# Kernel tuning notes

Hardware: AMD Instinct MI355X
Metric: run time of the kernel (lower is better)

## Reference

```python
import jax, jax.numpy as jnp
import numpy as np

H = 128
NH = 8
HD = H // NH  # 16
TANH_ALPHA = 10.0
LN_EPS = 1e-5


def _layer_norm(x, g, b):
    mu = jnp.mean(x, axis=-1, keepdims=True)
    var = jnp.mean((x - mu) ** 2, axis=-1, keepdims=True)
    return (x - mu) / jnp.sqrt(var + LN_EPS) * g + b


def setup_inputs() -> dict:
    key = jax.random.key(0)
    ks = jax.random.split(key, 24)
    B, N = 1024, 500

    def p(k, shape):
        return jax.random.normal(k, shape, dtype=jnp.float32) * 0.05

    inp = {
        "node_embeddings": jax.random.normal(ks[0], (B, N, H), jnp.float32),
        "graph_embeddings": jax.random.normal(ks[1], (B, H), jnp.float32),
        "first_node": jax.random.randint(ks[2], (B,), 0, N, jnp.int32),
        "current_node": jax.random.randint(ks[3], (B,), 0, N, jnp.int32),
        "mask": jax.random.randint(ks[4], (B, N), 0, 2, jnp.int32),
        # linear_first: Linear(384, 128)
        "W_first": p(ks[5], (H, 3 * H)),
        "b_first": p(ks[6], (H,)),
        # ln1 / ln2
        "g1": jnp.ones((H,), jnp.float32),
        "beta1": jnp.zeros((H,), jnp.float32),
        "g2": jnp.ones((H,), jnp.float32),
        "beta2": jnp.zeros((H,), jnp.float32),
        # LSTM(128,128) single layer, gate order i,f,g,o
        "W_ih": p(ks[7], (4 * H, H)),
        "W_hh": p(ks[8], (4 * H, H)),
        "b_ih": p(ks[9], (4 * H,)),
        "b_hh": p(ks[10], (4 * H,)),
        # attention / output projections (no bias)
        "Wq": p(ks[11], (H, H)),
        "Wk": p(ks[12], (H, H)),
        "Wv": p(ks[13], (H, H)),
        "Wproj": p(ks[14], (H, H)),
        # logitk: Linear(128,128) with bias
        "Wlk": p(ks[15], (H, H)),
        "blk": p(ks[16], (H,)),
    }
    return inp


def reference(node_embeddings, graph_embeddings, W_first, b_first, g1, beta1,
              W_ih, W_hh, b_ih, b_hh, g2, beta2, Wq, Wk, Wv, Wproj, Wlk, blk,
              first_node, current_node, mask):
    B, N, _ = node_embeddings.shape
    dt = node_embeddings.dtype

    # build_cache: K/V/logitK projections of all node embeddings
    ck = node_embeddings @ Wk.T                # [B,N,128]
    cv = node_embeddings @ Wv.T                # [B,N,128]
    lk = node_embeddings @ Wlk.T + blk         # [B,N,128]

    # context construction
    bidx = jnp.arange(B)
    first_emb = node_embeddings[bidx, first_node]    # [B,128]
    cur_emb = node_embeddings[bidx, current_node]    # [B,128]
    context = jnp.concatenate([graph_embeddings, first_emb, cur_emb], axis=1)
    context = _layer_norm(context @ W_first.T + b_first, g1, beta1)

    # single LSTM step from zero state (build_cache resets h,c to 0)
    gates = context @ W_ih.T + b_ih + b_hh           # h_prev = 0 -> no W_hh term
    i, f, g, o = jnp.split(gates, 4, axis=-1)
    c = jax.nn.sigmoid(i) * jnp.tanh(g)              # c_prev = 0
    h = jax.nn.sigmoid(o) * jnp.tanh(c)
    ctx = _layer_norm(h, g2, beta2)

    # multi-head single-query attention; note (e h) split: head is the FAST dim
    q = (ctx @ Wq.T).reshape(B, HD, NH).transpose(0, 2, 1)       # [B,h,e]
    k = ck.reshape(B, N, HD, NH).transpose(0, 3, 1, 2)           # [B,h,N,e]
    v = cv.reshape(B, N, HD, NH).transpose(0, 3, 1, 2)           # [B,h,N,e]
    maskf = mask.astype(dt)
    scores = jnp.einsum('bhe,bhne->bhn', q, k) / np.sqrt(HD) + maskf[:, None, :]
    att = jax.nn.softmax(scores, axis=-1)
    oh = jnp.einsum('bhn,bhne->bhe', att, v)                     # [B,h,e]
    att_out = oh.reshape(B, H)                                   # (h e): h slow, e fast

    context_emb = att_out @ Wproj.T                              # [B,128]
    comp = jnp.einsum('be,bne->bn', lk, context_emb[:, None, :].squeeze(1)[:, :][None].squeeze(0) if False else context_emb) if False else jnp.einsum('bne,be->bn', lk, context_emb)
    comp = comp / np.sqrt(H)
    comp = TANH_ALPHA * jnp.tanh(comp)
    out = jnp.where(mask == 1, -jnp.inf, comp)
    return out
```

## Files before the change

kernel.cpp:

```cpp
#include <hip/hip_runtime.h>
#include <math.h>

#define NBATCH 1024
#define NNODE  500
#define HDIM   128
#define NHEAD  8
#define G1K    2
#define SPLIT  2
#define CPB    4
#define CHUNK  64
#define PSTRIDE 1056
#define RSQRT_H 0.08838834764831845f
#define MASK_NEG (-1e30f)

__device__ __forceinline__ float wave_sum64(float v) {
    #pragma unroll
    for (int off = 32; off >= 1; off >>= 1) v += __shfl_xor(v, off, 64);
    return v;
}
__device__ __forceinline__ float wave_max64(float v) {
    #pragma unroll
    for (int off = 32; off >= 1; off >>= 1) v = fmaxf(v, __shfl_xor(v, off, 64));
    return v;
}

template<int G>
__device__ __forceinline__ void block_ln(float (&x)[G], const float* __restrict__ gw,
                                         const float* __restrict__ bw,
                                         int t, int lane, int wv, float (*wpart)[G])
{
    float s[G];
    #pragma unroll
    for (int g = 0; g < G; ++g) s[g] = x[g];
    #pragma unroll
    for (int off = 32; off >= 1; off >>= 1) {
        #pragma unroll
        for (int g = 0; g < G; ++g) s[g] += __shfl_xor(s[g], off, 64);
    }
    if (lane == 0) {
        #pragma unroll
        for (int g = 0; g < G; ++g) wpart[wv][g] = s[g];
    }
    __syncthreads();
    float mu[G];
    #pragma unroll
    for (int g = 0; g < G; ++g) mu[g] = (wpart[0][g] + wpart[1][g]) * (1.f/128.f);
    __syncthreads();
    #pragma unroll
    for (int g = 0; g < G; ++g) { float d = x[g] - mu[g]; s[g] = d * d; }
    #pragma unroll
    for (int off = 32; off >= 1; off >>= 1) {
        #pragma unroll
        for (int g = 0; g < G; ++g) s[g] += __shfl_xor(s[g], off, 64);
    }
    if (lane == 0) {
        #pragma unroll
        for (int g = 0; g < G; ++g) wpart[wv][g] = s[g];
    }
    __syncthreads();
    float gv = gw[t], bv = bw[t];
    #pragma unroll
    for (int g = 0; g < G; ++g) {
        float var = (wpart[0][g] + wpart[1][g]) * (1.f/128.f);
        x[g] = (x[g] - mu[g]) / sqrtf(var + 1e-5f) * gv + bv;
    }
    __syncthreads();
}

__global__ __launch_bounds__(128) void k1_context(
    const float* __restrict__ node, const float* __restrict__ graph,
    const int* __restrict__ firstn, const int* __restrict__ curn,
    const float* __restrict__ W_first, const float* __restrict__ b_first,
    const float* __restrict__ g1, const float* __restrict__ beta1,
    const float* __restrict__ W_ih, const float* __restrict__ b_ih,
    const float* __restrict__ b_hh, const float* __restrict__ g2,
    const float* __restrict__ beta2, const float* __restrict__ Wq,
    const float* __restrict__ Wk, float* __restrict__ qW_out)
{
    const int t = threadIdx.x;
    const int lane = t & 63, wv = t >> 6;
    const int b0 = blockIdx.x * G1K;
    __shared__ __align__(16) float ctx[G1K][384];
    __shared__ __align__(16) float bufB[G1K][128];
    __shared__ float wpart[2][G1K];

    #pragma unroll
    for (int g = 0; g < G1K; ++g) {
        int b = b0 + g;
        ctx[g][t]       = graph[b*HDIM + t];
        ctx[g][128 + t] = node[((size_t)b*NNODE + firstn[b])*HDIM + t];
        ctx[g][256 + t] = node[((size_t)b*NNODE + curn[b])*HDIM + t];
    }
    __syncthreads();

    float x[G1K];
    {
        const float4* Wf4 = (const float4*)W_first;
        float bf = b_first[t];
        #pragma unroll
        for (int g = 0; g < G1K; ++g) x[g] = bf;
        for (int j4 = 0; j4 < 96; ++j4) {
            float4 w = Wf4[t*96 + j4];
            #pragma unroll
            for (int g = 0; g < G1K; ++g) {
                float4 c = ((const float4*)ctx[g])[j4];
                x[g] += c.x*w.x + c.y*w.y + c.z*w.z + c.w*w.w;
            }
        }
    }
    block_ln<G1K>(x, g1, beta1, t, lane, wv, wpart);

    #pragma unroll
    for (int g = 0; g < G1K; ++g) bufB[g][t] = x[g];
    __syncthreads();

    float gi[G1K], gg[G1K], go[G1K];
    {
        const float4* Wih4 = (const float4*)W_ih;
        float bi = b_ih[t]       + b_hh[t];
        float bg = b_ih[256 + t] + b_hh[256 + t];
        float bo = b_ih[384 + t] + b_hh[384 + t];
        #pragma unroll
        for (int g = 0; g < G1K; ++g) { gi[g] = bi; gg[g] = bg; go[g] = bo; }
        for (int j4 = 0; j4 < 32; ++j4) {
            float4 wi = Wih4[(size_t)t*32 + j4];
            float4 wg = Wih4[(size_t)(256 + t)*32 + j4];
            float4 wo = Wih4[(size_t)(384 + t)*32 + j4];
            #pragma unroll
            for (int g = 0; g < G1K; ++g) {
                float4 v = ((const float4*)bufB[g])[j4];
                gi[g] += v.x*wi.x + v.y*wi.y + v.z*wi.z + v.w*wi.w;
                gg[g] += v.x*wg.x + v.y*wg.y + v.z*wg.z + v.w*wg.w;
                go[g] += v.x*wo.x + v.y*wo.y + v.z*wo.z + v.w*wo.w;
            }
        }
    }
    #pragma unroll
    for (int g = 0; g < G1K; ++g) {
        float ig = 1.f / (1.f + expf(-gi[g]));
        float cc = ig * tanhf(gg[g]);
        float og = 1.f / (1.f + expf(-go[g]));
        x[g] = og * tanhf(cc);
    }
    block_ln<G1K>(x, g2, beta2, t, lane, wv, wpart);

    #pragma unroll
    for (int g = 0; g < G1K; ++g) bufB[g][t] = x[g];
    __syncthreads();

    float q8[G1K];
    #pragma unroll
    for (int g = 0; g < G1K; ++g) q8[g] = 0.f;
    {
        const float4* Wq4 = (const float4*)Wq;
        for (int j4 = 0; j4 < 32; ++j4) {
            float4 w = Wq4[t*32 + j4];
            #pragma unroll
            for (int g = 0; g < G1K; ++g) {
                float4 v = ((const float4*)bufB[g])[j4];
                q8[g] += v.x*w.x + v.y*w.y + v.z*w.z + v.w*w.w;
            }
        }
    }
    __syncthreads();
    #pragma unroll
    for (int g = 0; g < G1K; ++g) bufB[g][t] = q8[g];
    __syncthreads();

    for (int h = 0; h < NHEAD; ++h) {
        float a[G1K];
        #pragma unroll
        for (int g = 0; g < G1K; ++g) a[g] = 0.f;
        for (int e = 0; e < 16; ++e) {
            float w = Wk[(e*8 + h)*HDIM + t];
            #pragma unroll
            for (int g = 0; g < G1K; ++g) a[g] += bufB[g][e*8 + h] * w;
        }
        #pragma unroll
        for (int g = 0; g < G1K; ++g)
            qW_out[((size_t)(b0 + g)*NHEAD + h)*HDIM + t] = 0.25f * a[g];
    }
}

__global__ __launch_bounds__(256) void k2a_reg(
    const float* __restrict__ node, const int* __restrict__ mask,
    const float* __restrict__ qW, float* __restrict__ part)
{
    const int b   = blockIdx.x >> 1;
    const int s   = blockIdx.x & (SPLIT - 1);
    const int tid = threadIdx.x;
    const int lane = tid & 63;
    const int wave = tid >> 6;
    const int nbase = s * (CPB * CHUNK);

    const int rn = tid >> 2;
    const int dq = tid & 3;
    const int sg = tid >> 5;
    const int aq = tid & 31;

    __shared__ __align__(16) float4 s_tile[CHUNK*32];
    __shared__ __align__(16) float  s_qw[NHEAD*HDIM];
    __shared__ float s_p[NHEAD*CHUNK];
    __shared__ float s_mask[CHUNK];
    __shared__ float s_m[NHEAD], s_l[NHEAD], s_c[NHEAD];

    const float* nodeb = node + (size_t)b*NNODE*HDIM;
    const int*   maskb = mask + (size_t)b*NNODE;

    float4 R[8];
    {
        int gn = nbase + rn;
        if (gn < NNODE) {
            const float4* src = (const float4*)(nodeb + (size_t)gn*HDIM) + dq*8;
            #pragma unroll
            for (int k = 0; k < 8; ++k) R[k] = src[k];
        } else {
            #pragma unroll
            for (int k = 0; k < 8; ++k) R[k] = make_float4(0.f,0.f,0.f,0.f);
        }
    }
    ((float4*)s_qw)[tid] = ((const float4*)(qW + (size_t)b*NHEAD*HDIM))[tid];
    if (tid < CHUNK) {
        int gn = nbase + tid;
        s_mask[tid] = (gn < NNODE) ? (float)maskb[gn] : 0.f;
    }
    if (tid < NHEAD) { s_m[tid] = -INFINITY; s_l[tid] = 0.f; }

    float4 acc[NHEAD];
    #pragma unroll
    for (int h = 0; h < NHEAD; ++h) acc[h] = make_float4(0.f,0.f,0.f,0.f);

    __syncthreads();

    for (int ck = 0; ck < CPB; ++ck) {
        const int base = nbase + ck*CHUNK;

        {
            float sc[NHEAD];
            #pragma unroll
            for (int h = 0; h < NHEAD; ++h) {
                const float4* qh = (const float4*)(s_qw + h*HDIM) + dq*8;
                float t0 = 0.f;
                #pragma unroll
                for (int k = 0; k < 8; ++k) {
                    float4 w = qh[k];
                    t0 += R[k].x*w.x + R[k].y*w.y + R[k].z*w.z + R[k].w*w.w;
                }
                sc[h] = t0;
            }
            #pragma unroll
            for (int h = 0; h < NHEAD; ++h) {
                sc[h] += __shfl_xor(sc[h], 1, 64);
                sc[h] += __shfl_xor(sc[h], 2, 64);
            }
            if (dq == 0) {
                int gn = base + rn;
                float mf = s_mask[rn];
                bool oob = (gn >= NNODE);
                #pragma unroll
                for (int h = 0; h < NHEAD; ++h)
                    s_p[h*64 + rn] = oob ? -INFINITY : sc[h] + mf;
            }
        }
        #pragma unroll
        for (int k = 0; k < 8; ++k) {
            int q = dq*8 + k;
            s_tile[rn*32 + (q ^ (rn & 31))] = R[k];
        }
        __syncthreads();

        for (int hh = wave; hh < NHEAD; hh += 4) {
            float sv = s_p[hh*64 + lane];
            float mx = wave_max64(sv);
            float mO = s_m[hh];
            float mN = fmaxf(mO, mx);
            float pv = __expf(sv - mN);
            s_p[hh*64 + lane] = pv;
            float sm = wave_sum64(pv);
            if (lane == 0) {
                float corr = __expf(mO - mN);
                s_c[hh] = corr;
                s_l[hh] = s_l[hh]*corr + sm;
                s_m[hh] = mN;
            }
        }
        __syncthreads();

        if (ck + 1 < CPB) {
            int gn = base + CHUNK + rn;
            if (gn < NNODE) {
                const float4* src = (const float4*)(nodeb + (size_t)gn*HDIM) + dq*8;
                #pragma unroll
                for (int k = 0; k < 8; ++k) R[k] = src[k];
            } else {
                #pragma unroll
                for (int k = 0; k < 8; ++k) R[k] = make_float4(0.f,0.f,0.f,0.f);
            }
            if (tid < CHUNK) {
                int gm = base + CHUNK + tid;
                s_mask[tid] = (gm < NNODE) ? (float)maskb[gm] : 0.f;
            }
        }

        {
            #pragma unroll
            for (int h = 0; h < NHEAD; ++h) {
                float c = s_c[h];
                acc[h].x *= c; acc[h].y *= c; acc[h].z *= c; acc[h].w *= c;
            }
            #pragma unroll
            for (int j = 0; j < 8; ++j) {
                int n = sg*8 + j;
                float4 nv = s_tile[n*32 + (aq ^ (n & 31))];
                #pragma unroll
                for (int h = 0; h < NHEAD; ++h) {
                    float p = s_p[h*64 + n];
                    acc[h].x += p*nv.x; acc[h].y += p*nv.y;
                    acc[h].z += p*nv.z; acc[h].w += p*nv.w;
                }
            }
        }
        __syncthreads();
    }

    float* pbase = part + (size_t)blockIdx.x * PSTRIDE;
    #pragma unroll
    for (int h = 0; h < NHEAD; ++h) s_tile[(sg*8 + h)*32 + aq] = acc[h];
    if (tid < NHEAD) { pbase[tid] = s_m[tid]; pbase[8 + tid] = s_l[tid]; }
    __syncthreads();
    {
        const int h2 = tid >> 5, q2 = tid & 31;
        float4 tot = make_float4(0.f,0.f,0.f,0.f);
        #pragma unroll
        for (int ss = 0; ss < 8; ++ss) {
            float4 v = s_tile[(ss*8 + h2)*32 + q2];
            tot.x += v.x; tot.y += v.y; tot.z += v.z; tot.w += v.w;
        }
        *(float4*)(pbase + 16 + h2*HDIM + q2*4) = tot;
    }
}

__global__ __launch_bounds__(256) void k2b_reduce(
    const float* __restrict__ part, const float* __restrict__ Wv,
    const float* __restrict__ Wproj, const float* __restrict__ Wlk,
    const float* __restrict__ blk, float* __restrict__ wce_out,
    float* __restrict__ bias_out)
{
    const int b = blockIdx.x;
    const int tid = threadIdx.x;
    __shared__ __align__(16) float s_an[NHEAD*HDIM];
    __shared__ float s_ao[HDIM], s_ce[HDIM];

    {
        const int h = tid >> 5, q = tid & 31;
        const float* pb = part + (size_t)b*SPLIT*PSTRIDE;
        float m[SPLIT], l[SPLIT];
        float gm = -INFINITY;
        #pragma unroll
        for (int s = 0; s < SPLIT; ++s) {
            m[s] = pb[s*PSTRIDE + h];
            l[s] = pb[s*PSTRIDE + 8 + h];
            gm = fmaxf(gm, m[s]);
        }
        float lsum = 0.f;
        float4 tot = make_float4(0.f,0.f,0.f,0.f);
        #pragma unroll
        for (int s = 0; s < SPLIT; ++s) {
            float f = __expf(m[s] - gm);
            lsum += l[s] * f;
            float4 v = *(const float4*)(pb + s*PSTRIDE + 16 + h*HDIM + q*4);
            tot.x += f*v.x; tot.y += f*v.y; tot.z += f*v.z; tot.w += f*v.w;
        }
        float inv = 1.f / lsum;
        tot.x *= inv; tot.y *= inv; tot.z *= inv; tot.w *= inv;
        *(float4*)(s_an + h*HDIM + q*4) = tot;
    }
    __syncthreads();

    if (tid < HDIM) {
        const int c = tid, h = c >> 4, e = c & 15;
        const int row = e*8 + h;
        float oh = 0.f;
        for (int d = 0; d < HDIM; ++d) oh += s_an[h*HDIM + d] * Wv[row*HDIM + d];
        s_ao[c] = oh;
    }
    __syncthreads();
    if (tid < HDIM) {
        const int c = tid;
        float ce = 0.f;
        for (int j = 0; j < HDIM; ++j) ce += s_ao[j] * Wproj[c*HDIM + j];
        s_ce[c] = ce;
    }
    __syncthreads();
    if (tid < HDIM) {
        const int d = tid;
        float w = 0.f;
        for (int c = 0; c < HDIM; ++c) w += s_ce[c] * Wlk[c*HDIM + d];
        wce_out[(size_t)b*HDIM + d] = w * RSQRT_H;
        if (d == 0) {
            float bb = 0.f;
            for (int c = 0; c < HDIM; ++c) bb += s_ce[c] * blk[c];
            bias_out[b] = bb * RSQRT_H;
        }
    }
}

__global__ __launch_bounds__(256) void k2_flash_mono(
    const float* __restrict__ node, const int* __restrict__ mask,
    const float* __restrict__ qW, const float* __restrict__ Wv,
    const float* __restrict__ Wproj, const float* __restrict__ Wlk,
    const float* __restrict__ blk, float* __restrict__ wce_out,
    float* __restrict__ bias_out)
{
    const int b = blockIdx.x;
    const int tid = threadIdx.x;
    const int lane = tid & 63;
    const int wave = tid >> 6;

    __shared__ float4 s_tile[64*32];
    __shared__ __align__(16) float s_qw[NHEAD*HDIM];
    __shared__ float  s_p[NHEAD*64];
    __shared__ float  s_m[NHEAD], s_l[NHEAD], s_c[NHEAD];
    __shared__ float  s_ao[HDIM], s_ce[HDIM];

    ((float4*)s_qw)[tid] = ((const float4*)(qW + (size_t)b*NHEAD*HDIM))[tid];
    if (tid < NHEAD) { s_m[tid] = -INFINITY; s_l[tid] = 0.f; }

    float4 acc[NHEAD];
    #pragma unroll
    for (int h = 0; h < NHEAD; ++h) acc[h] = make_float4(0.f,0.f,0.f,0.f);

    const int sn = tid & 63;
    const int hp = tid >> 6;
    const int sg = tid >> 5;
    const int aq = tid & 31;
    const float* nodeb = node + (size_t)b*NNODE*HDIM;

    for (int tile = 0; tile < 8; ++tile) {
        const int base = tile*64;
        #pragma unroll
        for (int i = 0; i < 8; ++i) {
            int idx = i*256 + tid;
            int r = idx >> 5, qq = idx & 31;
            int gn = base + r;
            float4 v = make_float4(0.f,0.f,0.f,0.f);
            if (gn < NNODE) v = *(const float4*)(nodeb + (size_t)gn*HDIM + qq*4);
            s_tile[r*32 + (qq ^ (r & 31))] = v;
        }
        __syncthreads();
        {
            float s0 = 0.f, s1 = 0.f;
            const int rb = sn*32, sw = sn & 31;
            const float4* qa = (const float4*)(s_qw + hp*HDIM);
            const float4* qb = (const float4*)(s_qw + (hp + 4)*HDIM);
            #pragma unroll 8
            for (int qq = 0; qq < 32; ++qq) {
                float4 nv = s_tile[rb + (qq ^ sw)];
                float4 av = qa[qq];
                float4 bv = qb[qq];
                s0 += nv.x*av.x + nv.y*av.y + nv.z*av.z + nv.w*av.w;
                s1 += nv.x*bv.x + nv.y*bv.y + nv.z*bv.z + nv.w*bv.w;
            }
            int gn = base + sn;
            if (gn < NNODE) {
                float mf = (float)mask[(size_t)b*NNODE + gn];
                s0 += mf; s1 += mf;
            } else { s0 = -INFINITY; s1 = -INFINITY; }
            s_p[hp*64 + sn] = s0;
            s_p[(hp + 4)*64 + sn] = s1;
        }
        __syncthreads();
        for (int hh = wave; hh < NHEAD; hh += 4) {
            float sv = s_p[hh*64 + lane];
            float mx = wave_max64(sv);
            float mO = s_m[hh];
            float mN = fmaxf(mO, mx);
            float pv = __expf(sv - mN);
            s_p[hh*64 + lane] = pv;
            float sm = wave_sum64(pv);
            if (lane == 0) {
                float corr = __expf(mO - mN);
                s_c[hh] = corr;
                s_l[hh] = s_l[hh]*corr + sm;
                s_m[hh] = mN;
            }
        }
        __syncthreads();
        {
            #pragma unroll
            for (int h = 0; h < NHEAD; ++h) {
                float c = s_c[h];
                acc[h].x *= c; acc[h].y *= c; acc[h].z *= c; acc[h].w *= c;
            }
            #pragma unroll
            for (int j = 0; j < 8; ++j) {
                int n = sg*8 + j;
                float4 nv = s_tile[n*32 + (aq ^ (n & 31))];
                #pragma unroll
                for (int h = 0; h < NHEAD; ++h) {
                    float p = s_p[h*64 + n];
                    acc[h].x += p*nv.x; acc[h].y += p*nv.y;
                    acc[h].z += p*nv.z; acc[h].w += p*nv.w;
                }
            }
        }
        __syncthreads();
    }
    #pragma unroll
    for (int h = 0; h < NHEAD; ++h) s_tile[(sg*8 + h)*32 + aq] = acc[h];
    __syncthreads();
    {
        const int h2 = tid >> 5, q2 = tid & 31;
        float4 tot = make_float4(0.f,0.f,0.f,0.f);
        #pragma unroll
        for (int s = 0; s < 8; ++s) {
            float4 v = s_tile[(s*8 + h2)*32 + q2];
            tot.x += v.x; tot.y += v.y; tot.z += v.z; tot.w += v.w;
        }
        float inv = 1.f / s_l[h2];
        tot.x *= inv; tot.y *= inv; tot.z *= inv; tot.w *= inv;
        ((float4*)s_qw)[h2*32 + q2] = tot;
    }
    __syncthreads();
    if (tid < HDIM) {
        const int c = tid, h = c >> 4, e = c & 15;
        const int row = e*8 + h;
        float oh = 0.f;
        for (int d = 0; d < HDIM; ++d) oh += s_qw[h*HDIM + d] * Wv[row*HDIM + d];
        s_ao[c] = oh;
    }
    __syncthreads();
    if (tid < HDIM) {
        const int c = tid;
        float ce = 0.f;
        for (int j = 0; j < HDIM; ++j) ce += s_ao[j] * Wproj[c*HDIM + j];
        s_ce[c] = ce;
    }
    __syncthreads();
    if (tid < HDIM) {
        const int d = tid;
        float w = 0.f;
        for (int c = 0; c < HDIM; ++c) w += s_ce[c] * Wlk[c*HDIM + d];
        wce_out[(size_t)b*HDIM + d] = w * RSQRT_H;
        if (d == 0) {
            float bb = 0.f;
            for (int c = 0; c < HDIM; ++c) bb += s_ce[c] * blk[c];
            bias_out[b] = bb * RSQRT_H;
        }
    }
}

__global__ __launch_bounds__(256) void k3_out(
    const float* __restrict__ node, const int* __restrict__ mask,
    const float* __restrict__ wce, const float* __restrict__ biasv,
    float* __restrict__ out)
{
    const int slot = (int)((blockIdx.x*256u + threadIdx.x) >> 5);
    const int q = threadIdx.x & 31;
    const int b = slot / NNODE;
    const float4 nv = *(const float4*)(node + (size_t)slot*HDIM + q*4);
    const float4 wv = *(const float4*)(wce + (size_t)b*HDIM + q*4);
    float p = nv.x*wv.x + nv.y*wv.y + nv.z*wv.z + nv.w*wv.w;
    #pragma unroll
    for (int off = 16; off >= 1; off >>= 1) p += __shfl_xor(p, off, 32);
    if (q == 0) {
        float v = 10.f * tanhf(p + biasv[b]);
        out[slot] = (mask[slot] == 1) ? MASK_NEG : v;
    }
}

extern "C" void kernel_launch(void* const* d_in, const int* in_sizes, int n_in,
                              void* d_out, int out_size, void* d_ws, size_t ws_size,
                              hipStream_t stream) {
    const float* node    = (const float*)d_in[0];
    const float* graph   = (const float*)d_in[1];
    const int*   firstn  = (const int*)d_in[2];
    const int*   curn    = (const int*)d_in[3];
    const int*   mask    = (const int*)d_in[4];
    const float* W_first = (const float*)d_in[5];
    const float* b_first = (const float*)d_in[6];
    const float* g1      = (const float*)d_in[7];
    const float* beta1   = (const float*)d_in[8];
    const float* g2      = (const float*)d_in[9];
    const float* beta2   = (const float*)d_in[10];
    const float* W_ih    = (const float*)d_in[11];
    const float* b_ih    = (const float*)d_in[13];
    const float* b_hh    = (const float*)d_in[14];
    const float* Wq      = (const float*)d_in[15];
    const float* Wk      = (const float*)d_in[16];
    const float* Wv      = (const float*)d_in[17];
    const float* Wproj   = (const float*)d_in[18];
    const float* Wlk     = (const float*)d_in[19];
    const float* blk     = (const float*)d_in[20];
    float* out = (float*)d_out;

    float* qW    = (float*)d_ws;
    float* wce   = qW + (size_t)NBATCH*NHEAD*HDIM;
    float* biasv = wce + (size_t)NBATCH*HDIM;
    float* part  = biasv + NBATCH;
    const size_t need = ((size_t)NBATCH*NHEAD*HDIM + (size_t)NBATCH*HDIM + NBATCH
                         + (size_t)NBATCH*SPLIT*PSTRIDE) * sizeof(float);

    k1_context<<<NBATCH/G1K, 128, 0, stream>>>(node, graph, firstn, curn,
        W_first, b_first, g1, beta1, W_ih, b_ih, b_hh, g2, beta2, Wq, Wk, qW);
    if (ws_size >= need) {
        k2a_reg<<<NBATCH*SPLIT, 256, 0, stream>>>(node, mask, qW, part);
        k2b_reduce<<<NBATCH, 256, 0, stream>>>(part, Wv, Wproj, Wlk, blk,
            wce, biasv);
    } else {
        k2_flash_mono<<<NBATCH, 256, 0, stream>>>(node, mask, qW, Wv, Wproj,
            Wlk, blk, wce, biasv);
    }
    k3_out<<<(NBATCH*NNODE)/8, 256, 0, stream>>>(node, mask, wce, biasv, out);
}
```

Before: 230.6 us.

## Split attention into 8 node chunks per batch with per-wave local softmax

The attention partial kernel now splits each batch into 8 blocks of 64 nodes rather than 2 blocks of 256. Each wave handles 16 nodes with its own in-register softmax and weighted sum, then the four waves are merged in shared memory. This drops the sequential chunk loop, the online-softmax rescaling and several block barriers, and launches four times as many blocks. The cost is more partial results written to memory and more merging work in the reduce kernel. The context kernel's batch grouping G1K also goes from 2 to 4.

```diff
diff --git a/kernel.cpp b/kernel.cpp
--- a/kernel.cpp
+++ b/kernel.cpp
@@ -5,11 +5,9 @@
 #define NNODE  500
 #define HDIM   128
 #define NHEAD  8
-#define G1K    2
-#define SPLIT  2
-#define CPB    4
-#define CHUNK  64
-#define PSTRIDE 1056
+#define G1K    4
+#define SPLIT  8
+#define PSTRIDE 1040
 #define RSQRT_H 0.08838834764831845f
 #define MASK_NEG (-1e30f)
 
@@ -182,161 +180,133 @@
     }
 }
 
-__global__ __launch_bounds__(256) void k2a_reg(
+__global__ __launch_bounds__(256) void k2a_wave(
     const float* __restrict__ node, const int* __restrict__ mask,
     const float* __restrict__ qW, float* __restrict__ part)
 {
-    const int b   = blockIdx.x >> 1;
-    const int s   = blockIdx.x & (SPLIT - 1);
+    const int b   = blockIdx.x >> 3;
+    const int s   = blockIdx.x & 7;
     const int tid = threadIdx.x;
+    const int w   = tid >> 6;
     const int lane = tid & 63;
-    const int wave = tid >> 6;
-    const int nbase = s * (CPB * CHUNK);
-
-    const int rn = tid >> 2;
-    const int dq = tid & 3;
-    const int sg = tid >> 5;
-    const int aq = tid & 31;
-
-    __shared__ __align__(16) float4 s_tile[CHUNK*32];
+    const int rnl = lane >> 2;
+    const int dq  = lane & 3;
+    const int gn  = s*64 + w*16 + rnl;
+
     __shared__ __align__(16) float  s_qw[NHEAD*HDIM];
-    __shared__ float s_p[NHEAD*CHUNK];
-    __shared__ float s_mask[CHUNK];
-    __shared__ float s_m[NHEAD], s_l[NHEAD], s_c[NHEAD];
-
-    const float* nodeb = node + (size_t)b*NNODE*HDIM;
-    const int*   maskb = mask + (size_t)b*NNODE;
+    __shared__ __align__(16) float4 s_tile[4][16*32];
+    __shared__ float s_pp[4][NHEAD*16];
+    __shared__ float s_ml[4][16];
+    __shared__ float s_gml[16];
+
+    ((float4*)s_qw)[tid] = ((const float4*)(qW + (size_t)b*NHEAD*HDIM))[tid];
 
     float4 R[8];
+    float mf = 0.f;
+    const bool valid = (gn < NNODE);
+    if (valid) {
+        const float4* src = (const float4*)(node + ((size_t)b*NNODE + gn)*HDIM) + dq*8;
+        #pragma unroll
+        for (int k = 0; k < 8; ++k) R[k] = src[k];
+        mf = (float)mask[(size_t)b*NNODE + gn];
+    } else {
+        #pragma unroll
+        for (int k = 0; k < 8; ++k) R[k] = make_float4(0.f,0.f,0.f,0.f);
+    }
+    __syncthreads();
+
+    float sc[NHEAD];
+    #pragma unroll
+    for (int h = 0; h < NHEAD; ++h) {
+        const float4* qh = (const float4*)(s_qw + h*HDIM) + dq*8;
+        float t0 = 0.f;
+        #pragma unroll
+        for (int k = 0; k < 8; ++k) {
+            float4 wv = qh[k];
+            t0 += R[k].x*wv.x + R[k].y*wv.y + R[k].z*wv.z + R[k].w*wv.w;
+        }
+        sc[h] = t0;
+    }
+    #pragma unroll
+    for (int h = 0; h < NHEAD; ++h) {
+        sc[h] += __shfl_xor(sc[h], 1, 64);
+        sc[h] += __shfl_xor(sc[h], 2, 64);
+        sc[h] = valid ? sc[h] + mf : -INFINITY;
+    }
+
+    float m[NHEAD], l[NHEAD], p[NHEAD];
+    #pragma unroll
+    for (int h = 0; h < NHEAD; ++h) {
+        float mx = sc[h];
+        #pragma unroll
+        for (int off = 4; off <= 32; off <<= 1) mx = fmaxf(mx, __shfl_xor(mx, off, 64));
+        m[h] = mx;
+        p[h] = __expf(sc[h] - mx);
+        float sm = p[h];
+        #pragma unroll
+        for (int off = 4; off <= 32; off <<= 1) sm += __shfl_xor(sm, off, 64);
+        l[h] = sm;
+    }
+
+    float4* tile = s_tile[w];
+    #pragma unroll
+    for (int k = 0; k < 8; ++k) {
+        int q = dq*8 + k;
+        tile[rnl*32 + (q ^ rnl)] = R[k];
+    }
+    if (dq == 0) {
+        #pragma unroll
+        for (int h = 0; h < NHEAD; ++h) s_pp[w][h*16 + rnl] = p[h];
+    }
+    if (lane == 0) {
+        #pragma unroll
+        for (int h = 0; h < NHEAD; ++h) { s_ml[w][h] = m[h]; s_ml[w][8 + h] = l[h]; }
+    }
+
+    float4 a4[4];
+    #pragma unroll
+    for (int j = 0; j < 4; ++j) a4[j] = make_float4(0.f,0.f,0.f,0.f);
+    const int h2 = lane >> 3, d16 = lane & 7;
+    #pragma unroll 4
+    for (int r = 0; r < 16; ++r) {
+        float pv = s_pp[w][h2*16 + r];
+        #pragma unroll
+        for (int j = 0; j < 4; ++j) {
+            float4 nv = tile[r*32 + ((d16*4 + j) ^ r)];
+            a4[j].x += pv*nv.x; a4[j].y += pv*nv.y;
+            a4[j].z += pv*nv.z; a4[j].w += pv*nv.w;
+        }
+    }
+    __syncthreads();
+
+    if (tid < NHEAD) {
+        float gm = -INFINITY;
+        #pragma unroll
+        for (int w4 = 0; w4 < 4; ++w4) gm = fmaxf(gm, s_ml[w4][tid]);
+        float lm = 0.f;
+        #pragma unroll
+        for (int w4 = 0; w4 < 4; ++w4)
+            lm += s_ml[w4][8 + tid] * __expf(s_ml[w4][tid] - gm);
+        s_gml[tid] = gm; s_gml[8 + tid] = lm;
+    }
+    #pragma unroll
+    for (int j = 0; j < 4; ++j)
+        ((float4*)s_tile)[w*256 + h2*32 + d16*4 + j] = a4[j];
+    __syncthreads();
+
+    float* pbase = part + (size_t)blockIdx.x * PSTRIDE;
     {
-        int gn = nbase + rn;
-        if (gn < NNODE) {
-            const float4* src = (const float4*)(nodeb + (size_t)gn*HDIM) + dq*8;
-            #pragma unroll
-            for (int k = 0; k < 8; ++k) R[k] = src[k];
-        } else {
-            #pragma unroll
-            for (int k = 0; k < 8; ++k) R[k] = make_float4(0.f,0.f,0.f,0.f);
-        }
-    }
-    ((float4*)s_qw)[tid] = ((const float4*)(qW + (size_t)b*NHEAD*HDIM))[tid];
-    if (tid < CHUNK) {
-        int gn = nbase + tid;
-        s_mask[tid] = (gn < NNODE) ? (float)maskb[gn] : 0.f;
-    }
-    if (tid < NHEAD) { s_m[tid] = -INFINITY; s_l[tid] = 0.f; }
-
-    float4 acc[NHEAD];
-    #pragma unroll
-    for (int h = 0; h < NHEAD; ++h) acc[h] = make_float4(0.f,0.f,0.f,0.f);
-
-    __syncthreads();
-
-    for (int ck = 0; ck < CPB; ++ck) {
-        const int base = nbase + ck*CHUNK;
-
-        {
-            float sc[NHEAD];
-            #pragma unroll
-            for (int h = 0; h < NHEAD; ++h) {
-                const float4* qh = (const float4*)(s_qw + h*HDIM) + dq*8;
-                float t0 = 0.f;
-                #pragma unroll
-                for (int k = 0; k < 8; ++k) {
-                    float4 w = qh[k];
-                    t0 += R[k].x*w.x + R[k].y*w.y + R[k].z*w.z + R[k].w*w.w;
-                }
-                sc[h] = t0;
-            }
-            #pragma unroll
-            for (int h = 0; h < NHEAD; ++h) {
-                sc[h] += __shfl_xor(sc[h], 1, 64);
-                sc[h] += __shfl_xor(sc[h], 2, 64);
-            }
-            if (dq == 0) {
-                int gn = base + rn;
-                float mf = s_mask[rn];
-                bool oob = (gn >= NNODE);
-                #pragma unroll
-                for (int h = 0; h < NHEAD; ++h)
-                    s_p[h*64 + rn] = oob ? -INFINITY : sc[h] + mf;
-            }
-        }
-        #pragma unroll
-        for (int k = 0; k < 8; ++k) {
-            int q = dq*8 + k;
-            s_tile[rn*32 + (q ^ (rn & 31))] = R[k];
-        }
-        __syncthreads();
-
-        for (int hh = wave; hh < NHEAD; hh += 4) {
-            float sv = s_p[hh*64 + lane];
-            float mx = wave_max64(sv);
-            float mO = s_m[hh];
-            float mN = fmaxf(mO, mx);
-            float pv = __expf(sv - mN);
-            s_p[hh*64 + lane] = pv;
-            float sm = wave_sum64(pv);
-            if (lane == 0) {
-                float corr = __expf(mO - mN);
-                s_c[hh] = corr;
-                s_l[hh] = s_l[hh]*corr + sm;
-                s_m[hh] = mN;
-            }
-        }
-        __syncthreads();
-
-        if (ck + 1 < CPB) {
-            int gn = base + CHUNK + rn;
-            if (gn < NNODE) {
-                const float4* src = (const float4*)(nodeb + (size_t)gn*HDIM) + dq*8;
-                #pragma unroll
-                for (int k = 0; k < 8; ++k) R[k] = src[k];
-            } else {
-                #pragma unroll
-                for (int k = 0; k < 8; ++k) R[k] = make_float4(0.f,0.f,0.f,0.f);
-            }
-            if (tid < CHUNK) {
-                int gm = base + CHUNK + tid;
-                s_mask[tid] = (gm < NNODE) ? (float)maskb[gm] : 0.f;
-            }
-        }
-
-        {
-            #pragma unroll
-            for (int h = 0; h < NHEAD; ++h) {
-                float c = s_c[h];
-                acc[h].x *= c; acc[h].y *= c; acc[h].z *= c; acc[h].w *= c;
-            }
-            #pragma unroll
-            for (int j = 0; j < 8; ++j) {
-                int n = sg*8 + j;
-                float4 nv = s_tile[n*32 + (aq ^ (n & 31))];
-                #pragma unroll
-                for (int h = 0; h < NHEAD; ++h) {
-                    float p = s_p[h*64 + n];
-                    acc[h].x += p*nv.x; acc[h].y += p*nv.y;
-                    acc[h].z += p*nv.z; acc[h].w += p*nv.w;
-                }
-            }
-        }
-        __syncthreads();
-    }
-
-    float* pbase = part + (size_t)blockIdx.x * PSTRIDE;
-    #pragma unroll
-    for (int h = 0; h < NHEAD; ++h) s_tile[(sg*8 + h)*32 + aq] = acc[h];
-    if (tid < NHEAD) { pbase[tid] = s_m[tid]; pbase[8 + tid] = s_l[tid]; }
-    __syncthreads();
-    {
-        const int h2 = tid >> 5, q2 = tid & 31;
+        const int hh = tid >> 5;
+        float gm = s_gml[hh];
         float4 tot = make_float4(0.f,0.f,0.f,0.f);
         #pragma unroll
-        for (int ss = 0; ss < 8; ++ss) {
-            float4 v = s_tile[(ss*8 + h2)*32 + q2];
-            tot.x += v.x; tot.y += v.y; tot.z += v.z; tot.w += v.w;
-        }
-        *(float4*)(pbase + 16 + h2*HDIM + q2*4) = tot;
+        for (int w4 = 0; w4 < 4; ++w4) {
+            float f = __expf(s_ml[w4][hh] - gm);
+            float4 v = ((float4*)s_tile)[w4*256 + tid];
+            tot.x += f*v.x; tot.y += f*v.y; tot.z += f*v.z; tot.w += f*v.w;
+        }
+        if (tid < 16) pbase[tid] = s_gml[tid];
+        *(float4*)(pbase + 16 + tid*4) = tot;
     }
 }
 
@@ -604,7 +574,7 @@
     k1_context<<<NBATCH/G1K, 128, 0, stream>>>(node, graph, firstn, curn,
         W_first, b_first, g1, beta1, W_ih, b_ih, b_hh, g2, beta2, Wq, Wk, qW);
     if (ws_size >= need) {
-        k2a_reg<<<NBATCH*SPLIT, 256, 0, stream>>>(node, mask, qW, part);
+        k2a_wave<<<NBATCH*SPLIT, 256, 0, stream>>>(node, mask, qW, part);
         k2b_reduce<<<NBATCH, 256, 0, stream>>>(part, Wv, Wproj, Wlk, blk,
             wce, biasv);
     } else {
```

Measured after the change: 245.5 us. 1.06x slower.
